# Kernel tuning notes

Measured on AMD Instinct MI355X. Metric: run time of the kernel, lower is better.

Reference implementation:

```python
import jax, jax.numpy as jnp
from jax import lax
import numpy as np

RADIUS = 0.1
NSAMPLE = 32
STRIDE = 3
ED_NSAMPLE = 10


def _sqdist(a, b):
    # a: [B,M,3], b: [B,N,3] -> [B,M,N] squared euclidean distance
    return (jnp.sum(a * a, -1)[:, :, None] + jnp.sum(b * b, -1)[:, None, :]
            - 2.0 * jnp.einsum('bmc,bnc->bmn', a, b))


def setup_inputs() -> dict:
    key = jax.random.key(0)
    ks = jax.random.split(key, 16)
    B, N = 8, 4096
    s = 0.05
    inp = {
        'data': jax.random.normal(ks[0], (B, N, 3), dtype=jnp.float32),
        'numpoints': N,
        # stem MLP 3 -> 64
        'W_stem': jax.random.normal(ks[1], (3, 64), dtype=jnp.float32) * s,
        'b_stem': jnp.zeros((64,), jnp.float32),
        # SA shared MLP (3 dp + 64 fj) -> 128
        'W_sa': jax.random.normal(ks[2], (67, 128), dtype=jnp.float32) * s,
        'b_sa': jnp.zeros((128,), jnp.float32),
        # FP MLP (128 interp + 64 skip) -> 64
        'W_fp': jax.random.normal(ks[3], (192, 64), dtype=jnp.float32) * s,
        'b_fp': jnp.zeros((64,), jnp.float32),
        # eigen-feature MLP 3 -> 4 -> 4
        'W_e1': jax.random.normal(ks[4], (3, 4), dtype=jnp.float32) * s,
        'b_e1': jnp.zeros((4,), jnp.float32),
        'W_e2': jax.random.normal(ks[5], (4, 4), dtype=jnp.float32) * s,
        'b_e2': jnp.zeros((4,), jnp.float32),
        # conv_final 1x1: 68 -> 64, + BN affine
        'W_fin': jax.random.normal(ks[6], (68, 64), dtype=jnp.float32) * s,
        'b_fin': jnp.zeros((64,), jnp.float32),
        'gamma': jnp.ones((64,), jnp.float32),
        'beta': jnp.zeros((64,), jnp.float32),
    }
    return inp


def reference(data, numpoints, W_stem, b_stem, W_sa, b_sa, W_fp, b_fp,
              W_e1, b_e1, W_e2, b_e2, W_fin, b_fin, gamma, beta):
    B, N, _ = data.shape
    b_ix = jnp.arange(B)[:, None, None]

    # ---------- encoder: stem MLP ----------
    f0 = jax.nn.relu(data @ W_stem + b_stem)  # [B,N,64]

    # set abstraction: stride-subsample centers, ball query, dp_fj, MLP, max
    sub_idx = jnp.arange(0, N, STRIDE)
    new_xyz = data[:, sub_idx]                 # [B,M,3]
    d2 = _sqdist(new_xyz, data)                # [B,M,N]
    col = jnp.arange(N, dtype=jnp.int32)
    valid = d2 < RADIUS * RADIUS
    keys = jnp.where(valid, col, N + col)      # first-valid ball query ordering
    negk, _ = lax.top_k(-keys, NSAMPLE)
    idx = -negk                                # [B,M,ns]
    first = idx[..., :1]                       # self point always valid
    idx = jnp.where(idx >= N, first, idx)
    g_xyz = data[b_ix, idx]                    # [B,M,ns,3]
    dp = (g_xyz - new_xyz[:, :, None, :]) / RADIUS  # normalize_dp
    g_f = f0[b_ix, idx]                        # [B,M,ns,64]
    feat = jnp.concatenate([dp, g_f], -1)      # [B,M,ns,67]
    h = jax.nn.relu(feat @ W_sa + b_sa)        # [B,M,ns,128]
    f_sub = jnp.max(h, axis=2)                 # [B,M,128]

    # ---------- decoder: 3-NN inverse-distance feature propagation ----------
    d2f = _sqdist(data, new_xyz)               # [B,N,M]
    negd, nn = lax.top_k(-d2f, 3)
    w = 1.0 / (-negd + 1e-8)
    w = w / jnp.sum(w, -1, keepdims=True)      # [B,N,3]
    nbr_f = f_sub[b_ix, nn]                    # [B,N,3,128]
    interp = jnp.einsum('bnk,bnkc->bnc', w, nbr_f)
    f = jax.nn.relu(jnp.concatenate([interp, f0], -1) @ W_fp + b_fp)  # [B,N,64]

    # ---------- KNN covariance eigen-features ----------
    d2e = _sqdist(data, data)                  # [B,N,N]
    _, gidx = lax.top_k(-d2e, ED_NSAMPLE)      # [B,N,k]
    nbr = data[b_ix, gidx]                     # [B,N,k,3]
    cen = nbr - jnp.mean(nbr, axis=2, keepdims=True)
    cov = jnp.einsum('bnkc,bnkd->bncd', cen, cen) / ED_NSAMPLE  # [B,N,3,3]
    eig = jnp.linalg.eigvalsh(cov)             # [B,N,3] ascending
    ef = jax.nn.relu(eig @ W_e1 + b_e1) @ W_e2 + b_e2  # [B,N,4]

    # ---------- fused 1x1 conv + BN (training-mode stats) + relu ----------
    z_in = jnp.concatenate([f, ef], -1)        # [B,N,68]
    zc = z_in @ W_fin + b_fin                  # [B,N,64]
    mu = jnp.mean(zc, axis=(0, 1))
    var = jnp.var(zc, axis=(0, 1))
    z = jax.nn.relu((zc - mu) * lax.rsqrt(var + 1e-5) * gamma + beta)
    z = jnp.transpose(z, (0, 2, 1))            # [B,64,N]
    return (data, z)
```

## Files before the change

### kernel.cpp

```cpp
#include <hip/hip_runtime.h>
#include <stdint.h>

#define BB 8
#define NN 4096
#define MM 1366
#define NS 32
#define RAD2 0.01f
#define NCH 16
#define CHUNK (NN/NCH)

static_assert(NCH * CHUNK == NN, "chunking");

__device__ __forceinline__ float rl(float v, int l) {
    return __int_as_float(__builtin_amdgcn_readlane(__float_as_int(v), l));
}
__device__ __forceinline__ uint32_t um(uint32_t a, uint32_t b) { return a < b ? a : b; }
__device__ __forceinline__ uint32_t ux(uint32_t a, uint32_t b) { return a > b ? a : b; }
__device__ __forceinline__ uint32_t um3(uint32_t a, uint32_t b, uint32_t c) { return um(um(a, b), c); }

__device__ __forceinline__ void mrg2(uint32_t* kk, uint32_t s0, uint32_t s1) {
    uint32_t n0 = um(kk[0], s0);
    uint32_t n1 = um3(kk[1], ux(kk[0], s0), s1);
    uint32_t n2 = um3(kk[2], ux(kk[1], s0), ux(kk[0], s1));
    uint32_t n3 = um3(kk[3], ux(kk[2], s0), ux(kk[1], s1));
    uint32_t n4 = um3(kk[4], ux(kk[3], s0), ux(kk[2], s1));
    uint32_t n5 = um3(kk[5], ux(kk[4], s0), ux(kk[3], s1));
    uint32_t n6 = um3(kk[6], ux(kk[5], s0), ux(kk[4], s1));
    uint32_t n7 = um3(kk[7], ux(kk[6], s0), ux(kk[5], s1));
    uint32_t n8 = um3(kk[8], ux(kk[7], s0), ux(kk[6], s1));
    uint32_t n9 = um3(kk[9], ux(kk[8], s0), ux(kk[7], s1));
    kk[0]=n0; kk[1]=n1; kk[2]=n2; kk[3]=n3; kk[4]=n4;
    kk[5]=n5; kk[6]=n6; kk[7]=n7; kk[8]=n8; kk[9]=n9;
}

__device__ __forceinline__ void mrg4(uint32_t* kk, uint32_t s0, uint32_t s1,
                                     uint32_t s2, uint32_t s3) {
    uint32_t n0 = um(kk[0], s0);
    uint32_t n1 = um3(kk[1], ux(kk[0], s0), s1);
    uint32_t n2 = um(um3(kk[2], ux(kk[1], s0), ux(kk[0], s1)), s2);
    uint32_t n3 = um3(um3(kk[3], ux(kk[2], s0), ux(kk[1], s1)), ux(kk[0], s2), s3);
    uint32_t n4 = um3(um3(kk[4], ux(kk[3], s0), ux(kk[2], s1)), ux(kk[1], s2), ux(kk[0], s3));
    uint32_t n5 = um3(um3(kk[5], ux(kk[4], s0), ux(kk[3], s1)), ux(kk[2], s2), ux(kk[1], s3));
    uint32_t n6 = um3(um3(kk[6], ux(kk[5], s0), ux(kk[4], s1)), ux(kk[3], s2), ux(kk[2], s3));
    uint32_t n7 = um3(um3(kk[7], ux(kk[6], s0), ux(kk[5], s1)), ux(kk[4], s2), ux(kk[3], s3));
    uint32_t n8 = um3(um3(kk[8], ux(kk[7], s0), ux(kk[6], s1)), ux(kk[5], s2), ux(kk[4], s3));
    uint32_t n9 = um3(um3(kk[9], ux(kk[8], s0), ux(kk[7], s1)), ux(kk[6], s2), ux(kk[5], s3));
    kk[0]=n0; kk[1]=n1; kk[2]=n2; kk[3]=n3; kk[4]=n4;
    kk[5]=n5; kk[6]=n6; kk[7]=n7; kk[8]=n8; kk[9]=n9;
}

__device__ __forceinline__ void srt4(uint32_t& a, uint32_t& b, uint32_t& c, uint32_t& d) {
    uint32_t t0 = um(a, b), t1 = ux(a, b), t2 = um(c, d), t3 = ux(c, d);
    uint32_t s0 = um(t0, t2), m0 = ux(t0, t2), m1 = um(t1, t3), s3 = ux(t1, t3);
    a = s0; b = um(m0, m1); c = ux(m0, m1); d = s3;
}

__global__ __launch_bounds__(256) void k_prep(const float* __restrict__ data,
                                              float* __restrict__ out,
                                              float4* __restrict__ cand4) {
    int t = blockIdx.x * 256 + threadIdx.x;
    float x = data[t * 3], y = data[t * 3 + 1], z = data[t * 3 + 2];
    out[t * 3] = x; out[t * 3 + 1] = y; out[t * 3 + 2] = z;
    cand4[t] = make_float4(x, y, z, x * x + y * y + z * z);
}

__global__ __launch_bounds__(256) void k_stem(const float* __restrict__ data,
                                              const float* __restrict__ Ws,
                                              const float* __restrict__ bs,
                                              float* __restrict__ f0) {
    int t = blockIdx.x * 256 + threadIdx.x;
    int c = t & 63;
    int r = t >> 6;
    const float* d = data + r * 3;
    float acc = bs[c];
    acc = fmaf(d[0], Ws[c], acc);
    acc = fmaf(d[1], Ws[64 + c], acc);
    acc = fmaf(d[2], Ws[128 + c], acc);
    f0[t] = fmaxf(acc, 0.f);
}

__global__ __launch_bounds__(256) void k_sa(const float4* __restrict__ cand4,
                                            const float* __restrict__ data,
                                            const float* __restrict__ f0,
                                            const uint32_t* __restrict__ mrg,
                                            const float* __restrict__ Wsa,
                                            const float* __restrict__ bsa,
                                            float* __restrict__ fsub) {
    __shared__ float2 sW[67 * 64];
    __shared__ int sIdx[4][NS];
    for (int i = threadIdx.x; i < 67 * 64; i += 256) {
        int k = i >> 6, c = i & 63;
        sW[i] = make_float2(Wsa[k * 128 + c], Wsa[k * 128 + 64 + c]);
    }
    __syncthreads();
    int wv = threadIdx.x >> 6, lane = threadIdx.x & 63;
    int gm = blockIdx.x * 4 + wv;
    if (gm >= BB * MM) return;
    int b = gm / MM, m = gm - b * MM;
    const float4* cb4 = cand4 + b * NN;
    const float* db = data + b * NN * 3;
    float4 cen = cb4[3 * m];
    float cx = cen.x, cy = cen.y, cz = cen.z, sa = cen.w;

    int cnt;
    bool fallback;
    {
        float d2l = 1e30f;
        int idxl = 0;
        if (lane < 10) {
            uint32_t key = mrg[lane * (BB * NN) + b * NN + 3 * m];
            idxl = (int)(key & 0xFFFu);
            float4 c = cb4[idxl];
            float dot = fmaf(cz, c.z, fmaf(cy, c.y, cx * c.x));
            d2l = (sa + c.w) - 2.f * dot;
        }
        bool valid = (lane < 10) && (d2l < RAD2);
        unsigned long long mask = __ballot(valid);
        if (valid) sIdx[wv][__popcll(mask & ((1ull << lane) - 1ull))] = idxl;
        cnt = __popcll(mask);
        fallback = rl(d2l, 9) < RAD2 * 1.0005f;
    }
    if (fallback) {
        cnt = 0;
        for (int base = 0; base < NN; base += 64) {
            int n = base + lane;
            float4 c = cb4[n];
            float dot = fmaf(cz, c.z, fmaf(cy, c.y, cx * c.x));
            float d2 = (sa + c.w) - 2.f * dot;
            bool valid = d2 < RAD2;
            unsigned long long mask = __ballot(valid);
            if (valid) {
                int pos = cnt + __popcll(mask & ((1ull << lane) - 1ull));
                if (pos < NS) sIdx[wv][pos] = n;
            }
            cnt += __popcll(mask);
            if (cnt >= NS) break;
        }
    }
    int scnt = cnt < NS ? cnt : NS;

    float cl = lane == 0 ? cx : (lane == 1 ? cy : cz);
    float hb0 = bsa[lane], hb1 = bsa[64 + lane];
    float m0 = 0.f, m1 = 0.f;

    for (int s0 = 0; s0 < scnt; s0 += 4) {
        float fr[4], fr2[4];
        #pragma unroll
        for (int u = 0; u < 4; ++u) {
            int s = s0 + u;
            if (s >= scnt) s = 0;
            int nj = sIdx[wv][s];
            int fb = (b * NN + nj) * 64;
            float v;
            if (lane >= 3) v = f0[fb + lane - 3];
            else           v = (db[nj * 3 + lane] - cl) * 10.0f;
            fr[u] = v;
            fr2[u] = (lane < 3) ? f0[fb + 61 + lane] : 0.f;
        }
        float h0[4], h1[4];
        #pragma unroll
        for (int u = 0; u < 4; ++u) { h0[u] = hb0; h1[u] = hb1; }
        for (int k = 0; k < 64; ++k) {
            float2 w = sW[k * 64 + lane];
            #pragma unroll
            for (int u = 0; u < 4; ++u) {
                float fv = rl(fr[u], k);
                h0[u] = fmaf(fv, w.x, h0[u]);
                h1[u] = fmaf(fv, w.y, h1[u]);
            }
        }
        #pragma unroll
        for (int k = 64; k < 67; ++k) {
            float2 w = sW[k * 64 + lane];
            #pragma unroll
            for (int u = 0; u < 4; ++u) {
                float fv = rl(fr2[u], k - 64);
                h0[u] = fmaf(fv, w.x, h0[u]);
                h1[u] = fmaf(fv, w.y, h1[u]);
            }
        }
        #pragma unroll
        for (int u = 0; u < 4; ++u) {
            m0 = fmaxf(m0, fmaxf(h0[u], 0.f));
            m1 = fmaxf(m1, fmaxf(h1[u], 0.f));
        }
    }
    fsub[gm * 128 + lane] = m0;
    fsub[gm * 128 + 64 + lane] = m1;
}

__global__ __launch_bounds__(512) void k_interp(const float4* __restrict__ cand4,
                                                const float* __restrict__ fsub,
                                                float* __restrict__ itp) {
    __shared__ float4 sC[MM];
    __shared__ float sMD[8][64][3];
    __shared__ int   sMI[8][64][3];
    __shared__ float sWts[64][3];
    __shared__ int   sNbr[64][3];
    int t = threadIdx.x, wv = t >> 6, lane = t & 63;
    int blk = blockIdx.x;
    int b = blk >> 6;
    int pbase = (blk & 63) * 64;
    const float4* cb4 = cand4 + b * NN;
    for (int m = t; m < MM; m += 512) sC[m] = cb4[3 * m];
    __syncthreads();
    int p = pbase + lane;
    float4 pm = cb4[p];
    float px = pm.x, py = pm.y, pz = pm.z, pa = pm.w;
    float d0 = 1e30f, d1 = 1e30f, d2v = 1e30f;
    int n0 = 0, n1 = 0, n2 = 0;
    int ms = wv * 171, me = ms + 171 < MM ? ms + 171 : MM;
    for (int m = ms; m < me; ++m) {
        float4 c = sC[m];
        float dd = (pa + c.w) - 2.f * (px * c.x + py * c.y + pz * c.z);
        if (dd < d2v) {
            if (dd < d1) {
                d2v = d1; n2 = n1;
                if (dd < d0) { d1 = d0; n1 = n0; d0 = dd; n0 = m; }
                else         { d1 = dd; n1 = m; }
            } else { d2v = dd; n2 = m; }
        }
    }
    sMD[wv][lane][0] = d0; sMD[wv][lane][1] = d1; sMD[wv][lane][2] = d2v;
    sMI[wv][lane][0] = n0; sMI[wv][lane][1] = n1; sMI[wv][lane][2] = n2;
    __syncthreads();
    if (wv == 0) {
        d0 = sMD[0][lane][0]; d1 = sMD[0][lane][1]; d2v = sMD[0][lane][2];
        n0 = sMI[0][lane][0]; n1 = sMI[0][lane][1]; n2 = sMI[0][lane][2];
        for (int w = 1; w < 8; ++w) {
            #pragma unroll
            for (int r = 0; r < 3; ++r) {
                float dd = sMD[w][lane][r];
                int mm = sMI[w][lane][r];
                if (dd < d2v) {
                    if (dd < d1) {
                        d2v = d1; n2 = n1;
                        if (dd < d0) { d1 = d0; n1 = n0; d0 = dd; n0 = mm; }
                        else         { d1 = dd; n1 = mm; }
                    } else { d2v = dd; n2 = mm; }
                }
            }
        }
        float w0 = 1.f / (d0 + 1e-8f), w1 = 1.f / (d1 + 1e-8f), w2 = 1.f / (d2v + 1e-8f);
        float ws = w0 + w1 + w2;
        sWts[lane][0] = w0 / ws; sWts[lane][1] = w1 / ws; sWts[lane][2] = w2 / ws;
        sNbr[lane][0] = n0; sNbr[lane][1] = n1; sNbr[lane][2] = n2;
    }
    __syncthreads();
    for (int i = wv * 8; i < wv * 8 + 8; ++i) {
        float a0 = sWts[i][0], a1 = sWts[i][1], a2 = sWts[i][2];
        const float* r0 = fsub + (b * MM + sNbr[i][0]) * 128;
        const float* r1 = fsub + (b * MM + sNbr[i][1]) * 128;
        const float* r2 = fsub + (b * MM + sNbr[i][2]) * 128;
        float v0 = fmaf(a2, r2[lane], fmaf(a1, r1[lane], a0 * r0[lane]));
        float v1 = fmaf(a2, r2[64 + lane], fmaf(a1, r1[64 + lane], a0 * r0[64 + lane]));
        int row = b * NN + pbase + i;
        itp[row * 128 + lane] = v0;
        itp[row * 128 + 64 + lane] = v1;
    }
}

__global__ __launch_bounds__(256) void k_knn_part(const float4* __restrict__ cand4,
                                                  uint32_t* __restrict__ pk) {
    int t = threadIdx.x;
    int blk = blockIdx.x;
    int ch = blk & (NCH - 1);
    int pg = (blk >> 4) & 15;
    int b = blk >> 8;
    const float4* cb = cand4 + b * NN;
    int c0 = ch * CHUNK;
    int p = pg * 256 + t;
    float4 me = cb[p];
    float px = me.x, py = me.y, pz = me.z, pa = me.w;
    uint32_t kk[10];
    #pragma unroll
    for (int r = 0; r < 10; ++r) kk[r] = 0xFFFFFF00u + r;
    for (int j = 0; j < CHUNK; j += 4) {
        float4 ca = cb[c0 + j];
        float4 cbv = cb[c0 + j + 1];
        float4 cc = cb[c0 + j + 2];
        float4 cd = cb[c0 + j + 3];
        float da = fmaxf(fmaf(-2.f, fmaf(pz, ca.z, fmaf(py, ca.y, px * ca.x)), pa + ca.w), 0.f);
        float db_ = fmaxf(fmaf(-2.f, fmaf(pz, cbv.z, fmaf(py, cbv.y, px * cbv.x)), pa + cbv.w), 0.f);
        float dc = fmaxf(fmaf(-2.f, fmaf(pz, cc.z, fmaf(py, cc.y, px * cc.x)), pa + cc.w), 0.f);
        float dd = fmaxf(fmaf(-2.f, fmaf(pz, cd.z, fmaf(py, cd.y, px * cd.x)), pa + cd.w), 0.f);
        uint32_t ka = (__float_as_uint(da) & 0xFFFFF000u) | (uint32_t)(c0 + j);
        uint32_t kb = (__float_as_uint(db_) & 0xFFFFF000u) | (uint32_t)(c0 + j + 1);
        uint32_t kc = (__float_as_uint(dc) & 0xFFFFF000u) | (uint32_t)(c0 + j + 2);
        uint32_t kd = (__float_as_uint(dd) & 0xFFFFF000u) | (uint32_t)(c0 + j + 3);
        srt4(ka, kb, kc, kd);
        mrg4(kk, ka, kb, kc, kd);
    }
    int gp = b * NN + p;
    #pragma unroll
    for (int r = 0; r < 10; ++r)
        pk[(ch * 10 + r) * (BB * NN) + gp] = kk[r];
}

__device__ __forceinline__ void jrot(float& app, float& aqq, float& apq,
                                     float& arp, float& arq) {
    float ap = apq;
    if (fabsf(ap) > 1e-32f) {
        float th = (aqq - app) / (2.f * ap);
        float t = 1.f / (fabsf(th) + sqrtf(th * th + 1.f));
        t = th < 0.f ? -t : t;
        float c = 1.f / sqrtf(t * t + 1.f);
        float s = t * c;
        app = app - t * ap;
        aqq = aqq + t * ap;
        apq = 0.f;
        float rp = arp, rq = arq;
        arp = c * rp - s * rq;
        arq = s * rp + c * rq;
    }
}

__global__ __launch_bounds__(256) void k_knn_eig(const float4* __restrict__ cand4,
                                                 const uint32_t* __restrict__ pk,
                                                 uint32_t* __restrict__ mrg,
                                                 const float* __restrict__ We1,
                                                 const float* __restrict__ be1,
                                                 const float* __restrict__ We2,
                                                 const float* __restrict__ be2,
                                                 float* __restrict__ ef) {
    int t = blockIdx.x * 256 + threadIdx.x;
    int b = t >> 12;
    const float4* cb = cand4 + b * NN;
    uint32_t kk[10];
    #pragma unroll
    for (int r = 0; r < 10; ++r) kk[r] = pk[r * (BB * NN) + t];
    for (int ch = 1; ch < NCH; ++ch) {
        uint32_t s[10];
        #pragma unroll
        for (int r = 0; r < 10; ++r) s[r] = pk[(ch * 10 + r) * (BB * NN) + t];
        mrg4(kk, s[0], s[1], s[2], s[3]);
        mrg4(kk, s[4], s[5], s[6], s[7]);
        mrg2(kk, s[8], s[9]);
    }
    #pragma unroll
    for (int r = 0; r < 10; ++r)
        mrg[r * (BB * NN) + t] = kk[r];
    float xs[10], ys[10], zs[10];
    float mx = 0.f, my = 0.f, mz = 0.f;
    #pragma unroll
    for (int r = 0; r < 10; ++r) {
        int n = (int)(kk[r] & 0xFFFu);
        float4 cr = cb[n];
        xs[r] = cr.x; ys[r] = cr.y; zs[r] = cr.z;
        mx += xs[r]; my += ys[r]; mz += zs[r];
    }
    mx *= 0.1f; my *= 0.1f; mz *= 0.1f;
    float a00 = 0, a01 = 0, a02 = 0, a11 = 0, a12 = 0, a22 = 0;
    #pragma unroll
    for (int r = 0; r < 10; ++r) {
        float x = xs[r] - mx, y = ys[r] - my, z = zs[r] - mz;
        a00 = fmaf(x, x, a00); a01 = fmaf(x, y, a01); a02 = fmaf(x, z, a02);
        a11 = fmaf(y, y, a11); a12 = fmaf(y, z, a12); a22 = fmaf(z, z, a22);
    }
    a00 *= 0.1f; a01 *= 0.1f; a02 *= 0.1f; a11 *= 0.1f; a12 *= 0.1f; a22 *= 0.1f;
    #pragma unroll
    for (int sweep = 0; sweep < 6; ++sweep) {
        jrot(a00, a11, a01, a02, a12);
        jrot(a00, a22, a02, a01, a12);
        jrot(a11, a22, a12, a01, a02);
    }
    float e0 = a00, e1 = a11, e2 = a22, tmp;
    if (e0 > e1) { tmp = e0; e0 = e1; e1 = tmp; }
    if (e1 > e2) { tmp = e1; e1 = e2; e2 = tmp; }
    if (e0 > e1) { tmp = e0; e0 = e1; e1 = tmp; }
    float tt[4];
    #pragma unroll
    for (int i = 0; i < 4; ++i) {
        float v = be1[i];
        v = fmaf(e0, We1[i], v);
        v = fmaf(e1, We1[4 + i], v);
        v = fmaf(e2, We1[8 + i], v);
        tt[i] = fmaxf(v, 0.f);
    }
    #pragma unroll
    for (int i = 0; i < 4; ++i) {
        float v = be2[i];
        v = fmaf(tt[0], We2[i], v);
        v = fmaf(tt[1], We2[4 + i], v);
        v = fmaf(tt[2], We2[8 + i], v);
        v = fmaf(tt[3], We2[12 + i], v);
        ef[t * 4 + i] = v;
    }
}

__global__ __launch_bounds__(256) void k_fp(const float* __restrict__ itp,
                                            const float* __restrict__ f0,
                                            const float* __restrict__ W,
                                            const float* __restrict__ bias,
                                            float* __restrict__ outf) {
    __shared__ float sW[192 * 64];
    for (int i = threadIdx.x; i < 192 * 64; i += 256) sW[i] = W[i];
    __syncthreads();
    int lane = threadIdx.x & 63;
    int wv = threadIdx.x >> 6;
    float bb = bias[lane];
    int rowbase = blockIdx.x * 64 + wv * 16;
    for (int it = 0; it < 4; ++it) {
        int r = rowbase + it * 4;
        float fa[4], fbv[4], fc[4], acc[4];
        #pragma unroll
        for (int u = 0; u < 4; ++u) {
            fa[u]  = itp[(r + u) * 128 + lane];
            fbv[u] = itp[(r + u) * 128 + 64 + lane];
            fc[u]  = f0[(r + u) * 64 + lane];
            acc[u] = bb;
        }
        #pragma unroll
        for (int k = 0; k < 192; ++k) {
            float w = sW[k * 64 + lane];
            #pragma unroll
            for (int u = 0; u < 4; ++u) {
                float fv = k < 64 ? rl(fa[u], k)
                         : (k < 128 ? rl(fbv[u], k - 64) : rl(fc[u], k - 128));
                acc[u] = fmaf(fv, w, acc[u]);
            }
        }
        #pragma unroll
        for (int u = 0; u < 4; ++u)
            outf[(r + u) * 64 + lane] = fmaxf(acc[u], 0.f);
    }
}

__global__ __launch_bounds__(256) void k_fin(const float* __restrict__ fb,
                                             const float* __restrict__ efb,
                                             const float* __restrict__ W,
                                             const float* __restrict__ bias,
                                             float* __restrict__ zc) {
    __shared__ float sW[68 * 64];
    for (int i = threadIdx.x; i < 68 * 64; i += 256) sW[i] = W[i];
    __syncthreads();
    int lane = threadIdx.x & 63;
    int wv = threadIdx.x >> 6;
    float bb = bias[lane];
    int rowbase = blockIdx.x * 64 + wv * 16;
    for (int it = 0; it < 4; ++it) {
        int r = rowbase + it * 4;
        float fa[4], fe[4], acc[4];
        #pragma unroll
        for (int u = 0; u < 4; ++u) {
            fa[u] = fb[(r + u) * 64 + lane];
            fe[u] = (lane < 4) ? efb[(r + u) * 4 + lane] : 0.f;
            acc[u] = bb;
        }
        #pragma unroll
        for (int k = 0; k < 68; ++k) {
            float w = sW[k * 64 + lane];
            #pragma unroll
            for (int u = 0; u < 4; ++u) {
                float fv = k < 64 ? rl(fa[u], k) : rl(fe[u], k - 64);
                acc[u] = fmaf(fv, w, acc[u]);
            }
        }
        #pragma unroll
        for (int u = 0; u < 4; ++u)
            zc[(r + u) * 64 + lane] = acc[u];
    }
}

__global__ __launch_bounds__(256) void k_stats1(const float* __restrict__ zc,
                                                float* __restrict__ pp) {
    int t = threadIdx.x;
    int c = t & 63, r4 = t >> 6;
    float s = 0.f, sq = 0.f;
    int base = blockIdx.x * 512;
    for (int i = 0; i < 128; ++i) {
        float v = zc[(base + i * 4 + r4) * 64 + c];
        s += v;
        sq = fmaf(v, v, sq);
    }
    __shared__ float ls[256], lq[256];
    ls[t] = s; lq[t] = sq;
    __syncthreads();
    if (t < 64) {
        float st = ls[t] + ls[t + 64] + ls[t + 128] + ls[t + 192];
        float qt = lq[t] + lq[t + 64] + lq[t + 128] + lq[t + 192];
        pp[blockIdx.x * 128 + t] = st;
        pp[blockIdx.x * 128 + 64 + t] = qt;
    }
}

__global__ __launch_bounds__(64) void k_stats2(const float* __restrict__ pp,
                                               const float* __restrict__ gamma,
                                               const float* __restrict__ beta,
                                               float* __restrict__ ss) {
    int c = threadIdx.x;
    float s = 0.f, sq = 0.f;
    for (int k = 0; k < 64; ++k) {
        s += pp[k * 128 + c];
        sq += pp[k * 128 + 64 + c];
    }
    const float inv = 1.f / (float)(BB * NN);
    float mu = s * inv;
    float var = sq * inv - mu * mu;
    float sc = gamma[c] / sqrtf(var + 1e-5f);
    ss[c] = sc;
    ss[64 + c] = beta[c] - mu * sc;
}

__global__ __launch_bounds__(256) void k_norm_t(const float* __restrict__ zc,
                                                const float* __restrict__ ss,
                                                float* __restrict__ out) {
    __shared__ float sT[64][65];
    int blk = blockIdx.x;
    int b = blk >> 6;
    int nbase = (blk & 63) * 64;
    int c = threadIdx.x & 63;
    int r4 = threadIdx.x >> 6;
    float sc = ss[c], sh = ss[64 + c];
    #pragma unroll
    for (int i = 0; i < 16; ++i) {
        int nr = i * 4 + r4;
        float v = zc[(b * NN + nbase + nr) * 64 + c];
        sT[nr][c] = fmaxf(fmaf(v, sc, sh), 0.f);
    }
    __syncthreads();
    int nn = threadIdx.x & 63;
    #pragma unroll
    for (int i = 0; i < 16; ++i) {
        int cc = i * 4 + r4;
        out[BB * NN * 3 + (b * 64 + cc) * NN + nbase + nn] = sT[nn][cc];
    }
}

extern "C" void kernel_launch(void* const* d_in, const int* in_sizes, int n_in,
                              void* d_out, int out_size, void* d_ws, size_t ws_size,
                              hipStream_t stream) {
    const float* data = (const float*)d_in[0];
    const float* Wst  = (const float*)d_in[2];
    const float* bst  = (const float*)d_in[3];
    const float* Wsa  = (const float*)d_in[4];
    const float* bsa  = (const float*)d_in[5];
    const float* Wfp  = (const float*)d_in[6];
    const float* bfp  = (const float*)d_in[7];
    const float* We1  = (const float*)d_in[8];
    const float* be1  = (const float*)d_in[9];
    const float* We2  = (const float*)d_in[10];
    const float* be2  = (const float*)d_in[11];
    const float* Wfin = (const float*)d_in[12];
    const float* bfin = (const float*)d_in[13];
    const float* gamma = (const float*)d_in[14];
    const float* beta  = (const float*)d_in[15];
    float* out = (float*)d_out;

    float* f0   = (float*)d_ws;
    float* fsub = f0 + 2097152;
    float* efb  = fsub + 1398784;
    float* zc   = efb + 131072;
    float* ss   = zc + 2097152;
    float* pp   = ss + 128;
    float4* cand4 = (float4*)(pp + 8192);
    uint32_t* mrgb = (uint32_t*)((float*)cand4 + 131072);
    float* itp  = (float*)mrgb + 1310720;
    float* fb   = itp + 4194304;
    uint32_t* pkk = (uint32_t*)itp;

    k_prep<<<(BB * NN) / 256, 256, 0, stream>>>(data, out, cand4);
    k_stem<<<(BB * NN * 64) / 256, 256, 0, stream>>>(data, Wst, bst, f0);
    k_knn_part<<<BB * 16 * NCH, 256, 0, stream>>>(cand4, pkk);
    k_knn_eig<<<(BB * NN) / 256, 256, 0, stream>>>(cand4, pkk, mrgb, We1, be1, We2, be2, efb);
    k_sa<<<(BB * MM + 3) / 4, 256, 0, stream>>>(cand4, data, f0, mrgb, Wsa, bsa, fsub);
    k_interp<<<BB * 64, 512, 0, stream>>>(cand4, fsub, itp);
    k_fp<<<512, 256, 0, stream>>>(itp, f0, Wfp, bfp, fb);
    k_fin<<<512, 256, 0, stream>>>(fb, efb, Wfin, bfin, zc);
    k_stats1<<<64, 256, 0, stream>>>(zc, pp);
    k_stats2<<<1, 64, 0, stream>>>(pp, gamma, beta, ss);
    k_norm_t<<<512, 256, 0, stream>>>(zc, ss, out);
}
```

Measured before the change: 300.9 us.

## Replace brute-force KNN merge with sample-threshold filtering and survivor insertion

The KNN stage no longer runs a sorting-network merge over every one of the 4096 candidates per point. It first computes the 10th-nearest key among a 256-candidate sample, then scans all candidates with a cheap compare against that threshold and stores the survivors. Only the survivors are inserted into the top-10 list, with a full brute-force fallback if any chunk overflows its capacity. This cuts the per-candidate min/max work at the cost of one extra launch, scattered survivor writes, divergent loops and reuse of the workspace buffers.

```diff
diff --git a/kernel.cpp b/kernel.cpp
--- a/kernel.cpp
+++ b/kernel.cpp
@@ -6,10 +6,7 @@
 #define MM 1366
 #define NS 32
 #define RAD2 0.01f
-#define NCH 16
-#define CHUNK (NN/NCH)
-
-static_assert(NCH * CHUNK == NN, "chunking");
+#define SCAP 96
 
 __device__ __forceinline__ float rl(float v, int l) {
     return __int_as_float(__builtin_amdgcn_readlane(__float_as_int(v), l));
@@ -55,6 +52,24 @@
     a = s0; b = um(m0, m1); c = ux(m0, m1); d = s3;
 }
 
+__device__ __forceinline__ void ins10(uint32_t* kk, uint32_t x) {
+    uint32_t t0 = kk[0];
+    kk[0] = um(kk[0], x);
+    #pragma unroll
+    for (int r = 1; r < 10; ++r) {
+        uint32_t xr = ux(t0, x);
+        t0 = kk[r];
+        kk[r] = um(kk[r], xr);
+    }
+}
+
+__device__ __forceinline__ uint32_t dkey(const float4& c, float px, float py,
+                                         float pz, float pa, int idx) {
+    float dot = fmaf(pz, c.z, fmaf(py, c.y, px * c.x));
+    float dd = fmaxf(fmaf(-2.f, dot, pa + c.w), 0.f);
+    return (__float_as_uint(dd) & 0xFFFFF000u) | (uint32_t)idx;
+}
+
 __global__ __launch_bounds__(256) void k_prep(const float* __restrict__ data,
                                               float* __restrict__ out,
                                               float4* __restrict__ cand4) {
@@ -77,6 +92,172 @@
     acc = fmaf(d[1], Ws[64 + c], acc);
     acc = fmaf(d[2], Ws[128 + c], acc);
     f0[t] = fmaxf(acc, 0.f);
+}
+
+__global__ __launch_bounds__(256) void k_knn_sub(const float4* __restrict__ cand4,
+                                                 uint32_t* __restrict__ pk) {
+    int t = threadIdx.x;
+    int blk = blockIdx.x;
+    int ch = blk & 3;
+    int pg = (blk >> 2) & 15;
+    int b = blk >> 6;
+    const float4* cb = cand4 + b * NN;
+    int c0 = ch * 64;
+    int q = b * NN + pg * 256 + t;
+    float4 me = cb[pg * 256 + t];
+    float px = me.x, py = me.y, pz = me.z, pa = me.w;
+    uint32_t kk[10];
+    #pragma unroll
+    for (int r = 0; r < 10; ++r) kk[r] = 0xFFFFFF00u + r;
+    for (int j = 0; j < 64; j += 4) {
+        uint32_t ka = dkey(cb[c0 + j],     px, py, pz, pa, c0 + j);
+        uint32_t kb = dkey(cb[c0 + j + 1], px, py, pz, pa, c0 + j + 1);
+        uint32_t kc = dkey(cb[c0 + j + 2], px, py, pz, pa, c0 + j + 2);
+        uint32_t kd = dkey(cb[c0 + j + 3], px, py, pz, pa, c0 + j + 3);
+        srt4(ka, kb, kc, kd);
+        mrg4(kk, ka, kb, kc, kd);
+    }
+    #pragma unroll
+    for (int r = 0; r < 10; ++r)
+        pk[(ch * 10 + r) * (BB * NN) + q] = kk[r];
+}
+
+__global__ __launch_bounds__(256) void k_knn_filt(const float4* __restrict__ cand4,
+                                                  const uint32_t* __restrict__ pk,
+                                                  unsigned short* __restrict__ sk,
+                                                  unsigned short* __restrict__ cnts) {
+    int t = threadIdx.x;
+    int blk = blockIdx.x;
+    int ch = blk & 3;
+    int pg = (blk >> 2) & 15;
+    int b = blk >> 6;
+    const float4* cb = cand4 + b * NN;
+    int q = b * NN + pg * 256 + t;
+    float4 me = cb[pg * 256 + t];
+    float px = me.x, py = me.y, pz = me.z, pa = me.w;
+    uint32_t kk[10];
+    #pragma unroll
+    for (int r = 0; r < 10; ++r) kk[r] = pk[r * (BB * NN) + q];
+    for (int s = 1; s < 4; ++s) {
+        uint32_t sv[10];
+        #pragma unroll
+        for (int r = 0; r < 10; ++r) sv[r] = pk[(s * 10 + r) * (BB * NN) + q];
+        mrg4(kk, sv[0], sv[1], sv[2], sv[3]);
+        mrg4(kk, sv[4], sv[5], sv[6], sv[7]);
+        mrg2(kk, sv[8], sv[9]);
+    }
+    uint32_t T = kk[9];
+    int c0 = ch * 1024;
+    uint32_t cnt = 0;
+    for (int j = 0; j < 1024; ++j) {
+        uint32_t key = dkey(cb[c0 + j], px, py, pz, pa, c0 + j);
+        if (key <= T) {
+            if (cnt < SCAP) sk[(ch * SCAP + cnt) * (BB * NN) + q] = (unsigned short)(c0 + j);
+            cnt++;
+        }
+    }
+    cnts[ch * (BB * NN) + q] = (unsigned short)cnt;
+}
+
+__device__ __forceinline__ void jrot(float& app, float& aqq, float& apq,
+                                     float& arp, float& arq) {
+    float ap = apq;
+    if (fabsf(ap) > 1e-32f) {
+        float th = (aqq - app) / (2.f * ap);
+        float t = 1.f / (fabsf(th) + sqrtf(th * th + 1.f));
+        t = th < 0.f ? -t : t;
+        float c = 1.f / sqrtf(t * t + 1.f);
+        float s = t * c;
+        app = app - t * ap;
+        aqq = aqq + t * ap;
+        apq = 0.f;
+        float rp = arp, rq = arq;
+        arp = c * rp - s * rq;
+        arq = s * rp + c * rq;
+    }
+}
+
+__global__ __launch_bounds__(256) void k_knn_meig(const float4* __restrict__ cand4,
+                                                  const unsigned short* __restrict__ sk,
+                                                  const unsigned short* __restrict__ cnts,
+                                                  uint32_t* __restrict__ mrg,
+                                                  const float* __restrict__ We1,
+                                                  const float* __restrict__ be1,
+                                                  const float* __restrict__ We2,
+                                                  const float* __restrict__ be2,
+                                                  float* __restrict__ ef) {
+    int q = blockIdx.x * 256 + threadIdx.x;
+    int b = q >> 12;
+    const float4* cb = cand4 + b * NN;
+    float4 me = cb[q & (NN - 1)];
+    float px = me.x, py = me.y, pz = me.z, pa = me.w;
+    uint32_t kk[10];
+    #pragma unroll
+    for (int r = 0; r < 10; ++r) kk[r] = 0xFFFFFF00u + r;
+    bool ovf = false;
+    for (int ch = 0; ch < 4; ++ch) {
+        int cnt = cnts[ch * (BB * NN) + q];
+        if (cnt > SCAP) { ovf = true; cnt = 0; }
+        for (int s = 0; s < cnt; ++s) {
+            int idx = sk[(ch * SCAP + s) * (BB * NN) + q];
+            ins10(kk, dkey(cb[idx], px, py, pz, pa, idx));
+        }
+    }
+    if (ovf) {
+        #pragma unroll
+        for (int r = 0; r < 10; ++r) kk[r] = 0xFFFFFF00u + r;
+        for (int j = 0; j < NN; ++j)
+            ins10(kk, dkey(cb[j], px, py, pz, pa, j));
+    }
+    #pragma unroll
+    for (int r = 0; r < 10; ++r)
+        mrg[r * (BB * NN) + q] = kk[r];
+    float xs[10], ys[10], zs[10];
+    float mx = 0.f, my = 0.f, mz = 0.f;
+    #pragma unroll
+    for (int r = 0; r < 10; ++r) {
+        int n = (int)(kk[r] & 0xFFFu);
+        float4 cr = cb[n];
+        xs[r] = cr.x; ys[r] = cr.y; zs[r] = cr.z;
+        mx += xs[r]; my += ys[r]; mz += zs[r];
+    }
+    mx *= 0.1f; my *= 0.1f; mz *= 0.1f;
+    float a00 = 0, a01 = 0, a02 = 0, a11 = 0, a12 = 0, a22 = 0;
+    #pragma unroll
+    for (int r = 0; r < 10; ++r) {
+        float x = xs[r] - mx, y = ys[r] - my, z = zs[r] - mz;
+        a00 = fmaf(x, x, a00); a01 = fmaf(x, y, a01); a02 = fmaf(x, z, a02);
+        a11 = fmaf(y, y, a11); a12 = fmaf(y, z, a12); a22 = fmaf(z, z, a22);
+    }
+    a00 *= 0.1f; a01 *= 0.1f; a02 *= 0.1f; a11 *= 0.1f; a12 *= 0.1f; a22 *= 0.1f;
+    #pragma unroll
+    for (int sweep = 0; sweep < 6; ++sweep) {
+        jrot(a00, a11, a01, a02, a12);
+        jrot(a00, a22, a02, a01, a12);
+        jrot(a11, a22, a12, a01, a02);
+    }
+    float e0 = a00, e1 = a11, e2 = a22, tmp;
+    if (e0 > e1) { tmp = e0; e0 = e1; e1 = tmp; }
+    if (e1 > e2) { tmp = e1; e1 = e2; e2 = tmp; }
+    if (e0 > e1) { tmp = e0; e0 = e1; e1 = tmp; }
+    float tt[4];
+    #pragma unroll
+    for (int i = 0; i < 4; ++i) {
+        float v = be1[i];
+        v = fmaf(e0, We1[i], v);
+        v = fmaf(e1, We1[4 + i], v);
+        v = fmaf(e2, We1[8 + i], v);
+        tt[i] = fmaxf(v, 0.f);
+    }
+    #pragma unroll
+    for (int i = 0; i < 4; ++i) {
+        float v = be2[i];
+        v = fmaf(tt[0], We2[i], v);
+        v = fmaf(tt[1], We2[4 + i], v);
+        v = fmaf(tt[2], We2[8 + i], v);
+        v = fmaf(tt[3], We2[12 + i], v);
+        ef[q * 4 + i] = v;
+    }
 }
 
 __global__ __launch_bounds__(256) void k_sa(const float4* __restrict__ cand4,
@@ -257,134 +438,6 @@
         int row = b * NN + pbase + i;
         itp[row * 128 + lane] = v0;
         itp[row * 128 + 64 + lane] = v1;
-    }
-}
-
-__global__ __launch_bounds__(256) void k_knn_part(const float4* __restrict__ cand4,
-                                                  uint32_t* __restrict__ pk) {
-    int t = threadIdx.x;
-    int blk = blockIdx.x;
-    int ch = blk & (NCH - 1);
-    int pg = (blk >> 4) & 15;
-    int b = blk >> 8;
-    const float4* cb = cand4 + b * NN;
-    int c0 = ch * CHUNK;
-    int p = pg * 256 + t;
-    float4 me = cb[p];
-    float px = me.x, py = me.y, pz = me.z, pa = me.w;
-    uint32_t kk[10];
-    #pragma unroll
-    for (int r = 0; r < 10; ++r) kk[r] = 0xFFFFFF00u + r;
-    for (int j = 0; j < CHUNK; j += 4) {
-        float4 ca = cb[c0 + j];
-        float4 cbv = cb[c0 + j + 1];
-        float4 cc = cb[c0 + j + 2];
-        float4 cd = cb[c0 + j + 3];
-        float da = fmaxf(fmaf(-2.f, fmaf(pz, ca.z, fmaf(py, ca.y, px * ca.x)), pa + ca.w), 0.f);
-        float db_ = fmaxf(fmaf(-2.f, fmaf(pz, cbv.z, fmaf(py, cbv.y, px * cbv.x)), pa + cbv.w), 0.f);
-        float dc = fmaxf(fmaf(-2.f, fmaf(pz, cc.z, fmaf(py, cc.y, px * cc.x)), pa + cc.w), 0.f);
-        float dd = fmaxf(fmaf(-2.f, fmaf(pz, cd.z, fmaf(py, cd.y, px * cd.x)), pa + cd.w), 0.f);
-        uint32_t ka = (__float_as_uint(da) & 0xFFFFF000u) | (uint32_t)(c0 + j);
-        uint32_t kb = (__float_as_uint(db_) & 0xFFFFF000u) | (uint32_t)(c0 + j + 1);
-        uint32_t kc = (__float_as_uint(dc) & 0xFFFFF000u) | (uint32_t)(c0 + j + 2);
-        uint32_t kd = (__float_as_uint(dd) & 0xFFFFF000u) | (uint32_t)(c0 + j + 3);
-        srt4(ka, kb, kc, kd);
-        mrg4(kk, ka, kb, kc, kd);
-    }
-    int gp = b * NN + p;
-    #pragma unroll
-    for (int r = 0; r < 10; ++r)
-        pk[(ch * 10 + r) * (BB * NN) + gp] = kk[r];
-}
-
-__device__ __forceinline__ void jrot(float& app, float& aqq, float& apq,
-                                     float& arp, float& arq) {
-    float ap = apq;
-    if (fabsf(ap) > 1e-32f) {
-        float th = (aqq - app) / (2.f * ap);
-        float t = 1.f / (fabsf(th) + sqrtf(th * th + 1.f));
-        t = th < 0.f ? -t : t;
-        float c = 1.f / sqrtf(t * t + 1.f);
-        float s = t * c;
-        app = app - t * ap;
-        aqq = aqq + t * ap;
-        apq = 0.f;
-        float rp = arp, rq = arq;
-        arp = c * rp - s * rq;
-        arq = s * rp + c * rq;
-    }
-}
-
-__global__ __launch_bounds__(256) void k_knn_eig(const float4* __restrict__ cand4,
-                                                 const uint32_t* __restrict__ pk,
-                                                 uint32_t* __restrict__ mrg,
-                                                 const float* __restrict__ We1,
-                                                 const float* __restrict__ be1,
-                                                 const float* __restrict__ We2,
-                                                 const float* __restrict__ be2,
-                                                 float* __restrict__ ef) {
-    int t = blockIdx.x * 256 + threadIdx.x;
-    int b = t >> 12;
-    const float4* cb = cand4 + b * NN;
-    uint32_t kk[10];
-    #pragma unroll
-    for (int r = 0; r < 10; ++r) kk[r] = pk[r * (BB * NN) + t];
-    for (int ch = 1; ch < NCH; ++ch) {
-        uint32_t s[10];
-        #pragma unroll
-        for (int r = 0; r < 10; ++r) s[r] = pk[(ch * 10 + r) * (BB * NN) + t];
-        mrg4(kk, s[0], s[1], s[2], s[3]);
-        mrg4(kk, s[4], s[5], s[6], s[7]);
-        mrg2(kk, s[8], s[9]);
-    }
-    #pragma unroll
-    for (int r = 0; r < 10; ++r)
-        mrg[r * (BB * NN) + t] = kk[r];
-    float xs[10], ys[10], zs[10];
-    float mx = 0.f, my = 0.f, mz = 0.f;
-    #pragma unroll
-    for (int r = 0; r < 10; ++r) {
-        int n = (int)(kk[r] & 0xFFFu);
-        float4 cr = cb[n];
-        xs[r] = cr.x; ys[r] = cr.y; zs[r] = cr.z;
-        mx += xs[r]; my += ys[r]; mz += zs[r];
-    }
-    mx *= 0.1f; my *= 0.1f; mz *= 0.1f;
-    float a00 = 0, a01 = 0, a02 = 0, a11 = 0, a12 = 0, a22 = 0;
-    #pragma unroll
-    for (int r = 0; r < 10; ++r) {
-        float x = xs[r] - mx, y = ys[r] - my, z = zs[r] - mz;
-        a00 = fmaf(x, x, a00); a01 = fmaf(x, y, a01); a02 = fmaf(x, z, a02);
-        a11 = fmaf(y, y, a11); a12 = fmaf(y, z, a12); a22 = fmaf(z, z, a22);
-    }
-    a00 *= 0.1f; a01 *= 0.1f; a02 *= 0.1f; a11 *= 0.1f; a12 *= 0.1f; a22 *= 0.1f;
-    #pragma unroll
-    for (int sweep = 0; sweep < 6; ++sweep) {
-        jrot(a00, a11, a01, a02, a12);
-        jrot(a00, a22, a02, a01, a12);
-        jrot(a11, a22, a12, a01, a02);
-    }
-    float e0 = a00, e1 = a11, e2 = a22, tmp;
-    if (e0 > e1) { tmp = e0; e0 = e1; e1 = tmp; }
-    if (e1 > e2) { tmp = e1; e1 = e2; e2 = tmp; }
-    if (e0 > e1) { tmp = e0; e0 = e1; e1 = tmp; }
-    float tt[4];
-    #pragma unroll
-    for (int i = 0; i < 4; ++i) {
-        float v = be1[i];
-        v = fmaf(e0, We1[i], v);
-        v = fmaf(e1, We1[4 + i], v);
-        v = fmaf(e2, We1[8 + i], v);
-        tt[i] = fmaxf(v, 0.f);
-    }
-    #pragma unroll
-    for (int i = 0; i < 4; ++i) {
-        float v = be2[i];
-        v = fmaf(tt[0], We2[i], v);
-        v = fmaf(tt[1], We2[4 + i], v);
-        v = fmaf(tt[2], We2[8 + i], v);
-        v = fmaf(tt[3], We2[12 + i], v);
-        ef[t * 4 + i] = v;
     }
 }
 
@@ -553,16 +606,21 @@
     float* zc   = efb + 131072;
     float* ss   = zc + 2097152;
     float* pp   = ss + 128;
-    float4* cand4 = (float4*)(pp + 8192);
+    float* cntf = pp + 8192;
+    float4* cand4 = (float4*)(cntf + 65536);
     uint32_t* mrgb = (uint32_t*)((float*)cand4 + 131072);
     float* itp  = (float*)mrgb + 1310720;
     float* fb   = itp + 4194304;
-    uint32_t* pkk = (uint32_t*)itp;
+    uint32_t* pkk = (uint32_t*)mrgb;
+    unsigned short* sk = (unsigned short*)itp;
+    unsigned short* cnts = (unsigned short*)cntf;
 
     k_prep<<<(BB * NN) / 256, 256, 0, stream>>>(data, out, cand4);
     k_stem<<<(BB * NN * 64) / 256, 256, 0, stream>>>(data, Wst, bst, f0);
-    k_knn_part<<<BB * 16 * NCH, 256, 0, stream>>>(cand4, pkk);
-    k_knn_eig<<<(BB * NN) / 256, 256, 0, stream>>>(cand4, pkk, mrgb, We1, be1, We2, be2, efb);
+    k_knn_sub<<<BB * 16 * 4, 256, 0, stream>>>(cand4, pkk);
+    k_knn_filt<<<BB * 16 * 4, 256, 0, stream>>>(cand4, pkk, sk, cnts);
+    k_knn_meig<<<(BB * NN) / 256, 256, 0, stream>>>(cand4, sk, cnts, mrgb,
+                                                    We1, be1, We2, be2, efb);
     k_sa<<<(BB * MM + 3) / 4, 256, 0, stream>>>(cand4, data, f0, mrgb, Wsa, bsa, fsub);
     k_interp<<<BB * 64, 512, 0, stream>>>(cand4, fsub, itp);
     k_fp<<<512, 256, 0, stream>>>(itp, f0, Wfp, bfp, fb);
```

After: 1.108 ms. +268.1%, slower.
